# Kernel optimization log

Measured on AMD Instinct MI355X. Metric: run time of the kernel, lower is better.

## Reference

```python
import jax, jax.numpy as jnp
import numpy as np

N, E, NB, P = 100000, 1600000, 1000, 500000


def gcn_conv(x, edge_index, W, b):
    # PyG GCNConv: add self-loops, symmetric D^-1/2 (A+I) D^-1/2 normalization,
    # linear transform, bias.
    n = x.shape[0]
    loop = jnp.arange(n, dtype=edge_index.dtype)
    src = jnp.concatenate([edge_index[0], loop])
    dst = jnp.concatenate([edge_index[1], loop])
    deg = jax.ops.segment_sum(jnp.ones(src.shape[0], x.dtype), dst, num_segments=n)
    dinv = jnp.where(deg > 0, jax.lax.rsqrt(deg), 0.0)
    norm = dinv[src] * dinv[dst]                       # [E+n]
    xw = x @ W                                          # [n, out]
    out = jax.ops.segment_sum(xw[src] * norm[:, None], dst, num_segments=n)
    return out + b


def setup_inputs() -> dict:
    key = jax.random.key(0)
    ks = jax.random.split(key, 12)
    x = jax.random.normal(ks[0], (N, 27), jnp.float32)
    edge_index = jax.random.randint(ks[1], (2, E), 0, N, dtype=jnp.int32)
    bank = jax.random.normal(ks[2], (NB, 27), jnp.float32)
    node1 = jax.random.randint(ks[3], (P,), 0, N + NB, dtype=jnp.int32)
    node2 = jax.random.randint(ks[4], (P,), 0, N + NB, dtype=jnp.int32)

    def lin(k, fan_in, fan_out):
        s = 1.0 / np.sqrt(fan_in)
        kw, kb = jax.random.split(k)
        W = jax.random.uniform(kw, (fan_in, fan_out), jnp.float32, -s, s)
        b = jax.random.uniform(kb, (fan_out,), jnp.float32, -s, s)
        return W, b

    W1, b1 = lin(ks[5], 27, 60)
    W2, b2 = lin(ks[6], 60, 50)
    Wb, bb = lin(ks[7], 27, 50)
    Wf1, bf1 = lin(ks[8], 100, 40)
    Wf2, bf2 = lin(ks[9], 40, 20)
    Wf3, bf3 = lin(ks[10], 20, 4)
    return dict(x=x, bank=bank, W1=W1, b1=b1, W2=W2, b2=b2, Wb=Wb, bb=bb,
                Wf1=Wf1, bf1=bf1, Wf2=Wf2, bf2=bf2, Wf3=Wf3, bf3=bf3,
                edge_index=edge_index, node1=node1, node2=node2)


def reference(x, bank, W1, b1, W2, b2, Wb, bb, Wf1, bf1, Wf2, bf2, Wf3, bf3,
              edge_index, node1, node2):
    h = gcn_conv(x, edge_index, W1, b1)                 # [N, 60]
    h = gcn_conv(h, edge_index, W2, b2)                 # [N, 50]
    bk = bank @ Wb + bb                                 # [NB, 50]
    allh = jnp.concatenate([h, bk], axis=0)             # [N+NB, 50]
    z = jnp.concatenate([allh[node1], allh[node2]], axis=1)  # [P, 100]
    z = z @ Wf1 + bf1
    z = z @ Wf2 + bf2
    z = z @ Wf3 + bf3                                   # [P, 4]
    return jax.nn.softmax(z, axis=0)                    # softmax over dim 0, as in source
```

## Files before the change

kernel.cpp:

```cpp
#include <hip/hip_runtime.h>
#include <math.h>

#define N_NODES 100000
#define N_EDGES 1600000
#define NB_BANK 1000
#define N_PAIRS 500000

#define BUCK_SHIFT 9
#define BUCK_NODES 512
#define NBUCK 196
#define BCAP 10240
#define EPB 16384
#define NSCAT 98
#define NZBLK 1954
#define SMASK 0x1FFFF

struct Consts {
  float C[27*8];
  float Rb[27*8];
  float u[8];
  float vg[8];
  float vb[8];
};

__device__ void precompute_body(
    const float* __restrict__ W1, const float* __restrict__ b1,
    const float* __restrict__ W2, const float* __restrict__ b2,
    const float* __restrict__ Wb, const float* __restrict__ bb,
    const float* __restrict__ Wf1, const float* __restrict__ bf1,
    const float* __restrict__ Wf2, const float* __restrict__ bf2,
    const float* __restrict__ Wf3, const float* __restrict__ bf3,
    Consts* __restrict__ cst) {
  __shared__ float A[40*4];
  __shared__ float T[100*4];
  __shared__ float B[60*8];
  __shared__ float cvec[4];
  const int tid = threadIdx.x;
  const int nt = blockDim.x;

  for (int idx = tid; idx < 160; idx += nt) {
    int r = idx >> 2, k = idx & 3;
    float s = 0.f;
    for (int j = 0; j < 20; ++j) s += Wf2[r*20+j] * Wf3[j*4+k];
    A[idx] = s;
  }
  __syncthreads();
  for (int idx = tid; idx < 400; idx += nt) {
    int r = idx >> 2, k = idx & 3;
    float s = 0.f;
    for (int j = 0; j < 40; ++j) s += Wf1[r*40+j] * A[j*4+k];
    T[idx] = s;
  }
  if (tid < 4) {
    float s = bf3[tid];
    for (int j = 0; j < 40; ++j) s += bf1[j] * A[j*4+tid];
    for (int j = 0; j < 20; ++j) s += bf2[j] * Wf3[j*4+tid];
    cvec[tid] = s;
  }
  __syncthreads();
  for (int idx = tid; idx < 480; idx += nt) {
    int r = idx >> 3, k = idx & 7;
    int half = k >> 2, kk = k & 3;
    float s = 0.f;
    for (int j = 0; j < 50; ++j) s += W2[r*50+j] * T[(half*50+j)*4+kk];
    B[idx] = s;
  }
  __syncthreads();
  for (int idx = tid; idx < 456; idx += nt) {
    if (idx < 216) {
      int r = idx >> 3, k = idx & 7;
      float s = 0.f;
      for (int j = 0; j < 60; ++j) s += W1[r*60+j] * B[j*8+k];
      cst->C[idx] = s;
    } else if (idx < 432) {
      int i2 = idx - 216;
      int r = i2 >> 3, k = i2 & 7, half = k >> 2, kk = k & 3;
      float s = 0.f;
      for (int j = 0; j < 50; ++j) s += Wb[r*50+j] * T[(half*50+j)*4+kk];
      cst->Rb[i2] = s;
    } else if (idx < 440) {
      int k = idx - 432;
      float s = 0.f;
      for (int j = 0; j < 60; ++j) s += b1[j] * B[j*8+k];
      cst->u[k] = s;
    } else if (idx < 448) {
      int k = idx - 440, half = k >> 2, kk = k & 3;
      float s = (half == 0) ? cvec[kk] : 0.f;
      for (int j = 0; j < 50; ++j) s += b2[j] * T[(half*50+j)*4+kk];
      cst->vg[k] = s;
    } else {
      int k = idx - 448, half = k >> 2, kk = k & 3;
      float s = (half == 0) ? cvec[kk] : 0.f;
      for (int j = 0; j < 50; ++j) s += bb[j] * T[(half*50+j)*4+kk];
      cst->vb[k] = s;
    }
  }
}

__global__ __launch_bounds__(1024) void k_scatter(
    const int* __restrict__ ei, int* __restrict__ bcnt, int* __restrict__ ebuf,
    const float* __restrict__ W1, const float* __restrict__ b1,
    const float* __restrict__ W2, const float* __restrict__ b2,
    const float* __restrict__ Wb, const float* __restrict__ bb,
    const float* __restrict__ Wf1, const float* __restrict__ bf1,
    const float* __restrict__ Wf2, const float* __restrict__ bf2,
    const float* __restrict__ Wf3, const float* __restrict__ bf3,
    Consts* __restrict__ cst) {
  if (blockIdx.x == NSCAT) {
    precompute_body(W1, b1, W2, b2, Wb, bb, Wf1, bf1, Wf2, bf2, Wf3, bf3, cst);
    return;
  }
  __shared__ int hist[NBUCK];
  __shared__ int base[NBUCK];
  const int t = threadIdx.x;
  const int e0 = blockIdx.x * EPB;
  if (t < NBUCK) hist[t] = 0;
  __syncthreads();
  for (int i = t; i < EPB; i += 1024) {
    int e = e0 + i;
    if (e < N_EDGES) atomicAdd(&hist[ei[N_EDGES + e] >> BUCK_SHIFT], 1);
  }
  __syncthreads();
  if (t < NBUCK) {
    int h = hist[t];
    base[t] = h ? (t * BCAP + atomicAdd(&bcnt[t], h)) : 0;
    hist[t] = 0;
  }
  __syncthreads();
  for (int i = t; i < EPB; i += 1024) {
    int e = e0 + i;
    if (e < N_EDGES) {
      int s = ei[e], d = ei[N_EDGES + e];
      int b = d >> BUCK_SHIFT;
      int pos = base[b] + atomicAdd(&hist[b], 1);
      ebuf[pos] = ((d & (BUCK_NODES - 1)) << 17) | s;
    }
  }
}

__global__ __launch_bounds__(512) void k_degfill(const int* __restrict__ bcnt,
                                                 const int* __restrict__ ebuf,
                                                 float* __restrict__ dinv,
                                                 int* __restrict__ rbeg,
                                                 int* __restrict__ rend,
                                                 int* __restrict__ csr) {
  __shared__ int cnt[BUCK_NODES];
  __shared__ int lcur[BUCK_NODES];
  const int b = blockIdx.x;
  const int t = threadIdx.x;
  cnt[t] = 0;
  __syncthreads();
  const int beg = b * BCAP, end = beg + bcnt[b];
  for (int j = beg + t; j < end; j += 512)
    atomicAdd(&cnt[ebuf[j] >> 17], 1);
  __syncthreads();
  int v = cnt[t];
  for (int off = 1; off < 512; off <<= 1) {
    int u = (t >= off) ? cnt[t - off] : 0;
    __syncthreads();
    cnt[t] += u;
    __syncthreads();
  }
  const int node = (b << BUCK_SHIFT) + t;
  const int excl = beg + cnt[t] - v;
  lcur[t] = excl;
  if (node < N_NODES) {
    rbeg[node] = excl;
    rend[node] = excl + v;
    dinv[node] = rsqrtf((float)v + 1.0f);
  }
  __syncthreads();
  for (int j = beg + t; j < end; j += 512) {
    int code = ebuf[j];
    int pos = atomicAdd(&lcur[code >> 17], 1);
    csr[pos] = code & SMASK;
  }
}

__global__ __launch_bounds__(256) void k_x8(const float* __restrict__ x,
                                            const float* __restrict__ dinv,
                                            const Consts* __restrict__ cst,
                                            float* __restrict__ Xs) {
  __shared__ float xs[32*27];
  const int tid = threadIdx.x;
  const int base = blockIdx.x * 32 * 27;
  for (int j = tid; j < 32*27; j += 256) {
    int g = base + j;
    xs[j] = (g < N_NODES*27) ? x[g] : 0.f;
  }
  __syncthreads();
  int li = tid >> 3, k = tid & 7;
  int node = blockIdx.x * 32 + li;
  if (node < N_NODES) {
    float s = 0.f;
    for (int c = 0; c < 27; ++c) s += xs[li*27+c] * cst->C[c*8+k];
    Xs[node*8+k] = s * dinv[node];
  }
}

__global__ __launch_bounds__(256) void k_gather1(const int* __restrict__ rbeg,
                                                 const int* __restrict__ rend,
                                                 const int* __restrict__ csr,
                                                 const float* __restrict__ dinv,
                                                 const float2* __restrict__ Xs2,
                                                 float2* __restrict__ Ys2,
                                                 float* __restrict__ dvec) {
  int t = blockIdx.x * 256 + threadIdx.x;
  int d = t >> 2, q = t & 3;
  if (d >= N_NODES) return;
  const int beg = rbeg[d], end = rend[d];
  const float nd = dinv[d];
  float2 self = Xs2[d*4 + q];
  float ax = self.x, ay = self.y;
  float dsum = nd;
  int j = beg;
  for (; j + 4 <= end; j += 4) {
    int s0 = csr[j], s1 = csr[j+1], s2 = csr[j+2], s3 = csr[j+3];
    float2 a0 = Xs2[s0*4+q], a1 = Xs2[s1*4+q], a2 = Xs2[s2*4+q], a3 = Xs2[s3*4+q];
    ax += (a0.x + a1.x) + (a2.x + a3.x);
    ay += (a0.y + a1.y) + (a2.y + a3.y);
    if (q == 0) dsum += (dinv[s0] + dinv[s1]) + (dinv[s2] + dinv[s3]);
  }
  for (; j < end; ++j) {
    int s = csr[j];
    float2 a = Xs2[s*4+q];
    ax += a.x; ay += a.y;
    if (q == 0) dsum += dinv[s];
  }
  float nn = nd * nd;
  Ys2[t] = make_float2(nn * ax, nn * ay);
  if (q == 0) dvec[d] = nd * dsum;
}

__global__ __launch_bounds__(256) void k_gather2g(const int* __restrict__ rbeg,
                                                  const int* __restrict__ rend,
                                                  const int* __restrict__ csr,
                                                  const float* __restrict__ dinv,
                                                  const float2* __restrict__ Ys2,
                                                  const float* __restrict__ dvec,
                                                  const float* __restrict__ bank,
                                                  const Consts* __restrict__ cst,
                                                  float2* __restrict__ gall2) {
  int t = blockIdx.x * 256 + threadIdx.x;
  int d = t >> 2, q = t & 3;
  if (d >= N_NODES + NB_BANK) return;
  int c0 = 2*q, c1 = 2*q + 1;
  if (d >= N_NODES) {
    int bk = d - N_NODES;
    float sx = cst->vb[c0], sy = cst->vb[c1];
    for (int cc = 0; cc < 27; ++cc) {
      float bv = bank[bk*27+cc];
      sx += bv * cst->Rb[cc*8+c0];
      sy += bv * cst->Rb[cc*8+c1];
    }
    gall2[t] = make_float2(sx, sy);
    return;
  }
  const int beg = rbeg[d], end = rend[d];
  float2 self = Ys2[d*4 + q];
  float ax = self.x, ay = self.y;
  int j = beg;
  for (; j + 4 <= end; j += 4) {
    int s0 = csr[j], s1 = csr[j+1], s2 = csr[j+2], s3 = csr[j+3];
    float2 a0 = Ys2[s0*4+q], a1 = Ys2[s1*4+q], a2 = Ys2[s2*4+q], a3 = Ys2[s3*4+q];
    ax += (a0.x + a1.x) + (a2.x + a3.x);
    ay += (a0.y + a1.y) + (a2.y + a3.y);
  }
  for (; j < end; ++j) {
    float2 a = Ys2[csr[j]*4+q];
    ax += a.x; ay += a.y;
  }
  float nd = dinv[d], dv = dvec[d];
  gall2[t] = make_float2(nd * ax + dv * cst->u[c0] + cst->vg[c0],
                         nd * ay + dv * cst->u[c1] + cst->vg[c1]);
}

__device__ inline void sm_merge(float4& m1, float4& s1,
                                const float4 m2, const float4 s2) {
  float4 M;
  M.x = fmaxf(m1.x, m2.x); M.y = fmaxf(m1.y, m2.y);
  M.z = fmaxf(m1.z, m2.z); M.w = fmaxf(m1.w, m2.w);
  s1.x = s1.x * expf(m1.x - M.x) + s2.x * expf(m2.x - M.x);
  s1.y = s1.y * expf(m1.y - M.y) + s2.y * expf(m2.y - M.y);
  s1.z = s1.z * expf(m1.z - M.z) + s2.z * expf(m2.z - M.z);
  s1.w = s1.w * expf(m1.w - M.w) + s2.w * expf(m2.w - M.w);
  m1 = M;
}

__global__ __launch_bounds__(256) void k_z(const int* __restrict__ node1,
                                           const int* __restrict__ node2,
                                           const float* __restrict__ gall,
                                           float* __restrict__ z,
                                           float4* __restrict__ bs_m,
                                           float4* __restrict__ bs_s) {
  int p = blockIdx.x * 256 + threadIdx.x;
  float4 m = make_float4(-1e30f, -1e30f, -1e30f, -1e30f);
  float4 s = make_float4(0.f, 0.f, 0.f, 0.f);
  if (p < N_PAIRS) {
    int n1 = node1[p], n2 = node2[p];
    const float4 a = *(const float4*)(gall + (size_t)n1*8);
    const float4 b = *(const float4*)(gall + (size_t)n2*8 + 4);
    float4 zv = make_float4(a.x+b.x, a.y+b.y, a.z+b.z, a.w+b.w);
    ((float4*)z)[p] = zv;
    m = zv; s = make_float4(1.f, 1.f, 1.f, 1.f);
  }
  __shared__ float4 lm[256], ls[256];
  lm[threadIdx.x] = m; ls[threadIdx.x] = s;
  __syncthreads();
  for (int st = 128; st > 0; st >>= 1) {
    if (threadIdx.x < st) {
      float4 mm = lm[threadIdx.x], ss = ls[threadIdx.x];
      sm_merge(mm, ss, lm[threadIdx.x + st], ls[threadIdx.x + st]);
      lm[threadIdx.x] = mm; ls[threadIdx.x] = ss;
    }
    __syncthreads();
  }
  if (threadIdx.x == 0) { bs_m[blockIdx.x] = lm[0]; bs_s[blockIdx.x] = ls[0]; }
}

__global__ __launch_bounds__(256) void k_comb(const float4* __restrict__ bs_m,
                                              const float4* __restrict__ bs_s,
                                              float* __restrict__ gms) {
  float4 m = make_float4(-1e30f, -1e30f, -1e30f, -1e30f);
  float4 s = make_float4(0.f, 0.f, 0.f, 0.f);
  for (int i = threadIdx.x; i < NZBLK; i += 256)
    sm_merge(m, s, bs_m[i], bs_s[i]);
  __shared__ float4 lm[256], ls[256];
  lm[threadIdx.x] = m; ls[threadIdx.x] = s;
  __syncthreads();
  for (int st = 128; st > 0; st >>= 1) {
    if (threadIdx.x < st) {
      float4 mm = lm[threadIdx.x], ss = ls[threadIdx.x];
      sm_merge(mm, ss, lm[threadIdx.x + st], ls[threadIdx.x + st]);
      lm[threadIdx.x] = mm; ls[threadIdx.x] = ss;
    }
    __syncthreads();
  }
  if (threadIdx.x == 0) {
    float4 M = lm[0], S = ls[0];
    gms[0] = M.x; gms[1] = M.y; gms[2] = M.z; gms[3] = M.w;
    gms[4] = S.x; gms[5] = S.y; gms[6] = S.z; gms[7] = S.w;
  }
}

__global__ __launch_bounds__(256) void k_final(const float* __restrict__ z,
                                               const float* __restrict__ gms,
                                               float* __restrict__ out) {
  int p = blockIdx.x * 256 + threadIdx.x;
  if (p < N_PAIRS) {
    float m0 = gms[0], m1 = gms[1], m2 = gms[2], m3 = gms[3];
    float i0 = 1.f / gms[4], i1 = 1.f / gms[5];
    float i2 = 1.f / gms[6], i3 = 1.f / gms[7];
    float4 zv = ((const float4*)z)[p];
    float4 o = make_float4(expf(zv.x - m0) * i0, expf(zv.y - m1) * i1,
                           expf(zv.z - m2) * i2, expf(zv.w - m3) * i3);
    ((float4*)out)[p] = o;
  }
}

extern "C" void kernel_launch(void* const* d_in, const int* in_sizes, int n_in,
                              void* d_out, int out_size, void* d_ws, size_t ws_size,
                              hipStream_t stream) {
  const float* x    = (const float*)d_in[0];
  const float* bank = (const float*)d_in[1];
  const float* W1   = (const float*)d_in[2];
  const float* b1   = (const float*)d_in[3];
  const float* W2   = (const float*)d_in[4];
  const float* b2   = (const float*)d_in[5];
  const float* Wb   = (const float*)d_in[6];
  const float* bb   = (const float*)d_in[7];
  const float* Wf1  = (const float*)d_in[8];
  const float* bf1  = (const float*)d_in[9];
  const float* Wf2  = (const float*)d_in[10];
  const float* bf2  = (const float*)d_in[11];
  const float* Wf3  = (const float*)d_in[12];
  const float* bf3  = (const float*)d_in[13];
  const int* ei     = (const int*)d_in[14];
  const int* node1  = (const int*)d_in[15];
  const int* node2  = (const int*)d_in[16];
  float* out = (float*)d_out;

  char* w = (char*)d_ws;
  size_t off = 0;
  auto take = [&](size_t bytes) -> char* {
    char* p = w + off;
    off = (off + bytes + 255) & ~(size_t)255;
    return p;
  };
  Consts* cst    = (Consts*)take(sizeof(Consts));
  int*    bcnt   = (int*)take(NBUCK * 4);
  float*  dinv   = (float*)take(N_NODES * 4);
  int*    rbeg   = (int*)take(N_NODES * 4);
  int*    rend   = (int*)take(N_NODES * 4);
  int*    csr    = (int*)take((size_t)NBUCK * BCAP * 4);
  float*  Xs     = (float*)take((size_t)N_NODES * 8 * 4);
  float*  Ys     = (float*)take((size_t)N_NODES * 8 * 4);
  float*  dvec   = (float*)take(N_NODES * 4);
  float*  gall   = (float*)take((size_t)(N_NODES + NB_BANK) * 8 * 4);
  char*   shreg  = take((size_t)NBUCK * BCAP * 4 > (size_t)N_PAIRS * 16
                        ? (size_t)NBUCK * BCAP * 4 : (size_t)N_PAIRS * 16);
  int*    ebuf   = (int*)shreg;
  float*  z      = (float*)shreg;
  float4* bs_m   = (float4*)take((size_t)NZBLK * 16);
  float4* bs_s   = (float4*)take((size_t)NZBLK * 16);
  float*  gms    = (float*)take(32);

  hipMemsetAsync(bcnt, 0, NBUCK * 4, stream);

  k_scatter<<<NSCAT + 1, 1024, 0, stream>>>(ei, bcnt, ebuf, W1, b1, W2, b2,
                                            Wb, bb, Wf1, bf1, Wf2, bf2,
                                            Wf3, bf3, cst);
  k_degfill<<<NBUCK, 512, 0, stream>>>(bcnt, ebuf, dinv, rbeg, rend, csr);
  k_x8<<<(N_NODES + 31) / 32, 256, 0, stream>>>(x, dinv, cst, Xs);
  k_gather1<<<(N_NODES * 4 + 255) / 256, 256, 0, stream>>>(
      rbeg, rend, csr, dinv, (const float2*)Xs, (float2*)Ys, dvec);
  k_gather2g<<<((N_NODES + NB_BANK) * 4 + 255) / 256, 256, 0, stream>>>(
      rbeg, rend, csr, dinv, (const float2*)Ys, dvec, bank, cst, (float2*)gall);
  k_z<<<NZBLK, 256, 0, stream>>>(node1, node2, gall, z, bs_m, bs_s);
  k_comb<<<1, 256, 0, stream>>>(bs_m, bs_s, gms);
  k_final<<<NZBLK, 256, 0, stream>>>(z, gms, out);
}
```

Measured before the change: 209.5 us.

## Spread edge scatter over more blocks, widen degfill, unroll gathers by eight

The edge scatter now uses 4096 edges per block across 391 blocks, up from 98, so more CUs take part. Each thread keeps its destination indices in registers so they are not reloaded in the second pass. The degree/CSR fill kernel goes from 512 to 1024 threads per block, and both neighbor-gather loops are unrolled to 8 to keep more loads in flight. In exchange, more blocks contend on the global bucket-counter atomics, and the wider unroll adds register pressure.

```diff
diff --git a/kernel.cpp b/kernel.cpp
--- a/kernel.cpp
+++ b/kernel.cpp
@@ -10,8 +10,8 @@
 #define BUCK_NODES 512
 #define NBUCK 196
 #define BCAP 10240
-#define EPB 16384
-#define NSCAT 98
+#define EPB 4096
+#define NSCAT 391
 #define NZBLK 1954
 #define SMASK 0x1FFFF
 
@@ -114,11 +114,15 @@
   __shared__ int base[NBUCK];
   const int t = threadIdx.x;
   const int e0 = blockIdx.x * EPB;
+  int dcache[EPB / 1024];
   if (t < NBUCK) hist[t] = 0;
   __syncthreads();
-  for (int i = t; i < EPB; i += 1024) {
-    int e = e0 + i;
-    if (e < N_EDGES) atomicAdd(&hist[ei[N_EDGES + e] >> BUCK_SHIFT], 1);
+#pragma unroll
+  for (int i = 0; i < EPB / 1024; ++i) {
+    int e = e0 + i * 1024 + t;
+    int d = (e < N_EDGES) ? ei[N_EDGES + e] : -1;
+    dcache[i] = d;
+    if (d >= 0) atomicAdd(&hist[d >> BUCK_SHIFT], 1);
   }
   __syncthreads();
   if (t < NBUCK) {
@@ -127,10 +131,12 @@
     hist[t] = 0;
   }
   __syncthreads();
-  for (int i = t; i < EPB; i += 1024) {
-    int e = e0 + i;
-    if (e < N_EDGES) {
-      int s = ei[e], d = ei[N_EDGES + e];
+#pragma unroll
+  for (int i = 0; i < EPB / 1024; ++i) {
+    int e = e0 + i * 1024 + t;
+    int d = dcache[i];
+    if (d >= 0) {
+      int s = ei[e];
       int b = d >> BUCK_SHIFT;
       int pos = base[b] + atomicAdd(&hist[b], 1);
       ebuf[pos] = ((d & (BUCK_NODES - 1)) << 17) | s;
@@ -138,39 +144,41 @@
   }
 }
 
-__global__ __launch_bounds__(512) void k_degfill(const int* __restrict__ bcnt,
-                                                 const int* __restrict__ ebuf,
-                                                 float* __restrict__ dinv,
-                                                 int* __restrict__ rbeg,
-                                                 int* __restrict__ rend,
-                                                 int* __restrict__ csr) {
+__global__ __launch_bounds__(1024) void k_degfill(const int* __restrict__ bcnt,
+                                                  const int* __restrict__ ebuf,
+                                                  float* __restrict__ dinv,
+                                                  int* __restrict__ rbeg,
+                                                  int* __restrict__ rend,
+                                                  int* __restrict__ csr) {
   __shared__ int cnt[BUCK_NODES];
   __shared__ int lcur[BUCK_NODES];
   const int b = blockIdx.x;
   const int t = threadIdx.x;
-  cnt[t] = 0;
+  if (t < BUCK_NODES) cnt[t] = 0;
   __syncthreads();
   const int beg = b * BCAP, end = beg + bcnt[b];
-  for (int j = beg + t; j < end; j += 512)
+  for (int j = beg + t; j < end; j += 1024)
     atomicAdd(&cnt[ebuf[j] >> 17], 1);
   __syncthreads();
-  int v = cnt[t];
-  for (int off = 1; off < 512; off <<= 1) {
-    int u = (t >= off) ? cnt[t - off] : 0;
+  int v = (t < BUCK_NODES) ? cnt[t] : 0;
+  for (int off = 1; off < BUCK_NODES; off <<= 1) {
+    int u = (t < BUCK_NODES && t >= off) ? cnt[t - off] : 0;
     __syncthreads();
-    cnt[t] += u;
+    if (t < BUCK_NODES) cnt[t] += u;
     __syncthreads();
   }
-  const int node = (b << BUCK_SHIFT) + t;
-  const int excl = beg + cnt[t] - v;
-  lcur[t] = excl;
-  if (node < N_NODES) {
-    rbeg[node] = excl;
-    rend[node] = excl + v;
-    dinv[node] = rsqrtf((float)v + 1.0f);
-  }
-  __syncthreads();
-  for (int j = beg + t; j < end; j += 512) {
+  if (t < BUCK_NODES) {
+    const int node = (b << BUCK_SHIFT) + t;
+    const int excl = beg + cnt[t] - v;
+    lcur[t] = excl;
+    if (node < N_NODES) {
+      rbeg[node] = excl;
+      rend[node] = excl + v;
+      dinv[node] = rsqrtf((float)v + 1.0f);
+    }
+  }
+  __syncthreads();
+  for (int j = beg + t; j < end; j += 1024) {
     int code = ebuf[j];
     int pos = atomicAdd(&lcur[code >> 17], 1);
     csr[pos] = code & SMASK;
@@ -214,12 +222,16 @@
   float ax = self.x, ay = self.y;
   float dsum = nd;
   int j = beg;
-  for (; j + 4 <= end; j += 4) {
-    int s0 = csr[j], s1 = csr[j+1], s2 = csr[j+2], s3 = csr[j+3];
+  for (; j + 8 <= end; j += 8) {
+    int s0 = csr[j],   s1 = csr[j+1], s2 = csr[j+2], s3 = csr[j+3];
+    int s4 = csr[j+4], s5 = csr[j+5], s6 = csr[j+6], s7 = csr[j+7];
     float2 a0 = Xs2[s0*4+q], a1 = Xs2[s1*4+q], a2 = Xs2[s2*4+q], a3 = Xs2[s3*4+q];
-    ax += (a0.x + a1.x) + (a2.x + a3.x);
-    ay += (a0.y + a1.y) + (a2.y + a3.y);
-    if (q == 0) dsum += (dinv[s0] + dinv[s1]) + (dinv[s2] + dinv[s3]);
+    float2 a4 = Xs2[s4*4+q], a5 = Xs2[s5*4+q], a6 = Xs2[s6*4+q], a7 = Xs2[s7*4+q];
+    ax += ((a0.x + a1.x) + (a2.x + a3.x)) + ((a4.x + a5.x) + (a6.x + a7.x));
+    ay += ((a0.y + a1.y) + (a2.y + a3.y)) + ((a4.y + a5.y) + (a6.y + a7.y));
+    if (q == 0)
+      dsum += ((dinv[s0] + dinv[s1]) + (dinv[s2] + dinv[s3]))
+            + ((dinv[s4] + dinv[s5]) + (dinv[s6] + dinv[s7]));
   }
   for (; j < end; ++j) {
     int s = csr[j];
@@ -260,11 +272,13 @@
   float2 self = Ys2[d*4 + q];
   float ax = self.x, ay = self.y;
   int j = beg;
-  for (; j + 4 <= end; j += 4) {
-    int s0 = csr[j], s1 = csr[j+1], s2 = csr[j+2], s3 = csr[j+3];
+  for (; j + 8 <= end; j += 8) {
+    int s0 = csr[j],   s1 = csr[j+1], s2 = csr[j+2], s3 = csr[j+3];
+    int s4 = csr[j+4], s5 = csr[j+5], s6 = csr[j+6], s7 = csr[j+7];
     float2 a0 = Ys2[s0*4+q], a1 = Ys2[s1*4+q], a2 = Ys2[s2*4+q], a3 = Ys2[s3*4+q];
-    ax += (a0.x + a1.x) + (a2.x + a3.x);
-    ay += (a0.y + a1.y) + (a2.y + a3.y);
+    float2 a4 = Ys2[s4*4+q], a5 = Ys2[s5*4+q], a6 = Ys2[s6*4+q], a7 = Ys2[s7*4+q];
+    ax += ((a0.x + a1.x) + (a2.x + a3.x)) + ((a4.x + a5.x) + (a6.x + a7.x));
+    ay += ((a0.y + a1.y) + (a2.y + a3.y)) + ((a4.y + a5.y) + (a6.y + a7.y));
   }
   for (; j < end; ++j) {
     float2 a = Ys2[csr[j]*4+q];
@@ -410,7 +424,7 @@
   k_scatter<<<NSCAT + 1, 1024, 0, stream>>>(ei, bcnt, ebuf, W1, b1, W2, b2,
                                             Wb, bb, Wf1, bf1, Wf2, bf2,
                                             Wf3, bf3, cst);
-  k_degfill<<<NBUCK, 512, 0, stream>>>(bcnt, ebuf, dinv, rbeg, rend, csr);
+  k_degfill<<<NBUCK, 1024, 0, stream>>>(bcnt, ebuf, dinv, rbeg, rend, csr);
   k_x8<<<(N_NODES + 31) / 32, 256, 0, stream>>>(x, dinv, cst, Xs);
   k_gather1<<<(N_NODES * 4 + 255) / 256, 256, 0, stream>>>(
       rbeg, rend, csr, dinv, (const float2*)Xs, (float2*)Ys, dvec);
```

New measurement: 203.1 us, median of 2. -3.0%, faster.
